# Optimization experiments

Measured on AMD Instinct MI355X. Metric: run time of the kernel, lower is better.

Reference implementation:

```python
import jax, jax.numpy as jnp
import numpy as np

N, E, D_IN, D_H, D_OUT = 100000, 1600000, 128, 128, 47
BN_EPS = 1e-5


def setup_inputs() -> dict:
    key = jax.random.key(0)
    ks = jax.random.split(key, 12)
    x = jax.random.normal(ks[0], (N, D_IN), dtype=jnp.float32)
    edge_index = jax.random.randint(ks[1], (2, E), 0, N, dtype=jnp.int64)
    s = 1.0 / np.sqrt(D_H)
    return {
        "x": x,
        "edge_index": edge_index,
        "W1": jax.random.normal(ks[2], (D_IN, D_H), dtype=jnp.float32) * s,
        "b1": jnp.zeros((D_H,), dtype=jnp.float32),
        "gamma": jax.random.uniform(ks[3], (D_H,), dtype=jnp.float32, minval=0.5, maxval=1.5),
        "beta": jax.random.normal(ks[4], (D_H,), dtype=jnp.float32) * 0.1,
        "mean": jax.random.normal(ks[5], (D_H,), dtype=jnp.float32) * 0.1,
        "var": jax.random.uniform(ks[6], (D_H,), dtype=jnp.float32, minval=0.5, maxval=1.5),
        "W2": jax.random.normal(ks[7], (D_H, D_H), dtype=jnp.float32) * s,
        "b2": jnp.zeros((D_H,), dtype=jnp.float32),
        "Wf": jax.random.normal(ks[8], (D_H, D_OUT), dtype=jnp.float32) * s,
        "bf": jnp.zeros((D_OUT,), dtype=jnp.float32),
    }


def gcn_conv(x, src, dst, W, b, n):
    # x' = x @ W, then symmetric-normalized aggregation with self-loops (PyG GCNConv).
    h = x @ W
    loops = jnp.arange(n, dtype=src.dtype)
    s = jnp.concatenate([src, loops])
    d = jnp.concatenate([dst, loops])
    deg = jax.ops.segment_sum(jnp.ones_like(d, dtype=h.dtype), d, num_segments=n)
    dinv = jnp.where(deg > 0, jax.lax.rsqrt(deg), 0.0)
    norm = dinv[s] * dinv[d]                      # [E+N]
    msg = h[s] * norm[:, None]                    # [E+N, D] gather
    out = jax.ops.segment_sum(msg, d, num_segments=n)  # scatter-add
    return out + b


def reference(x, edge_index, W1, b1, gamma, beta, mean, var, W2, b2, Wf, bf):
    n = x.shape[0]
    src, dst = edge_index[0], edge_index[1]
    # layer 1: GCNConv -> BatchNorm (eval) -> ReLU -> dropout (identity in eval)
    h1 = gcn_conv(x, src, dst, W1, b1, n)
    h1 = (h1 - mean) * jax.lax.rsqrt(var + BN_EPS) * gamma + beta
    h1 = jax.nn.relu(h1)
    # layer 2 (last conv, no BN/act)
    h2 = gcn_conv(h1, src, dst, W2, b2, n)
    # JumpingKnowledge max over layer outputs
    jk = jnp.maximum(h1, h2)
    logits = jk @ Wf + bf
    return jax.nn.log_softmax(logits, axis=1)
```

## Files before the change

kernel.cpp:

```cpp
#include <hip/hip_runtime.h>
#include <math.h>

#define DH 128
#define DOUT 47
#define BN_EPS 1e-5f

typedef __attribute__((ext_vector_type(8))) short short8;
typedef __attribute__((ext_vector_type(4))) float float4v;

__device__ __forceinline__ unsigned bf16_rne(float f) {
    unsigned u = __float_as_uint(f);
    return (u + 0x7fffu + ((u >> 16) & 1u)) >> 16;
}
__device__ __forceinline__ unsigned pack_bf2(float a, float b) {
    return (bf16_rne(a) & 0xffffu) | (bf16_rne(b) << 16);
}
__device__ __forceinline__ float2 unpack_bf2(unsigned u) {
    return make_float2(__uint_as_float(u << 16),
                       __uint_as_float(u & 0xffff0000u));
}


__global__ void zero_int_k(int* __restrict__ p, int n) {
    int i = blockIdx.x * 256 + threadIdx.x;
    if (i < n) p[i] = 0;
}

__global__ __launch_bounds__(256) void count_rank_k(const int* __restrict__ dst,
                                                    int* __restrict__ counts,
                                                    int* __restrict__ rank, int e) {
    int i0 = (blockIdx.x * 256 + threadIdx.x) * 4;
    if (i0 + 4 <= e) {
        int4 d4 = *(const int4*)(dst + i0);
        int4 r4;
        r4.x = atomicAdd(&counts[d4.x], 1);
        r4.y = atomicAdd(&counts[d4.y], 1);
        r4.z = atomicAdd(&counts[d4.z], 1);
        r4.w = atomicAdd(&counts[d4.w], 1);
        *(int4*)(rank + i0) = r4;
    } else {
        for (int i = i0; i < e; i++) rank[i] = atomicAdd(&counts[dst[i]], 1);
    }
}

__global__ __launch_bounds__(256) void scan1_k(const int* __restrict__ counts,
                                               int* __restrict__ offsets,
                                               int* __restrict__ blocksums, int n) {
    __shared__ int sd[256];
    int tid = threadIdx.x;
    int base = blockIdx.x * 1024 + tid * 4;
    int v0 = (base + 0 < n) ? ((counts[base + 0] + 7) & ~7) : 0;
    int v1 = (base + 1 < n) ? ((counts[base + 1] + 7) & ~7) : 0;
    int v2 = (base + 2 < n) ? ((counts[base + 2] + 7) & ~7) : 0;
    int v3 = (base + 3 < n) ? ((counts[base + 3] + 7) & ~7) : 0;
    int tsum = v0 + v1 + v2 + v3;
    sd[tid] = tsum;
    __syncthreads();
    for (int off = 1; off < 256; off <<= 1) {
        int x = (tid >= off) ? sd[tid - off] : 0;
        __syncthreads();
        sd[tid] += x;
        __syncthreads();
    }
    if (tid == 255) blocksums[blockIdx.x] = sd[255];
    int run = sd[tid] - tsum;
    if (base + 0 < n) offsets[base + 0] = run;  run += v0;
    if (base + 1 < n) offsets[base + 1] = run;  run += v1;
    if (base + 2 < n) offsets[base + 2] = run;  run += v2;
    if (base + 3 < n) offsets[base + 3] = run;
}

__global__ __launch_bounds__(128) void scan2_k(int* __restrict__ blocksums, int nb) {
    __shared__ int sd[128];
    int tid = threadIdx.x;
    int v = (tid < nb) ? blocksums[tid] : 0;
    sd[tid] = v;
    __syncthreads();
    for (int off = 1; off < 128; off <<= 1) {
        int x = (tid >= off) ? sd[tid - off] : 0;
        __syncthreads();
        sd[tid] += x;
        __syncthreads();
    }
    if (tid < nb) blocksums[tid] = sd[tid] - v;
}

__global__ void finalize_k(int* __restrict__ offsets,
                           float* __restrict__ dinv, const int* __restrict__ counts,
                           const int* __restrict__ blocksums,
                           int2* __restrict__ ew, int n) {
    int i = blockIdx.x * 256 + threadIdx.x;
    if (i >= n) return;
    int o = offsets[i] + blocksums[i >> 10];
    offsets[i] = o;
    int c = counts[i];
    dinv[i] = rsqrtf((float)(c + 1));
    int cP = (c + 7) & ~7;
    int2 z; z.x = 0; z.y = 0;
    for (int j = o + c; j < o + cP; ++j) ew[j] = z;
}

__global__ __launch_bounds__(256) void scatter_k(const int* __restrict__ src,
                                                 const int* __restrict__ dst,
                                                 const int* __restrict__ rank,
                                                 const int* __restrict__ offsets,
                                                 const float* __restrict__ dinv,
                                                 int2* __restrict__ ew, int e) {
    int i0 = (blockIdx.x * 256 + threadIdx.x) * 4;
    if (i0 + 4 <= e) {
        int4 s4 = *(const int4*)(src + i0);
        int4 d4 = *(const int4*)(dst + i0);
        int4 r4 = *(const int4*)(rank + i0);
        int sa[4] = {s4.x, s4.y, s4.z, s4.w};
        int da[4] = {d4.x, d4.y, d4.z, d4.w};
        int ra[4] = {r4.x, r4.y, r4.z, r4.w};
        int slot[4];
        float w[4];
#pragma unroll
        for (int k = 0; k < 4; k++) slot[k] = offsets[da[k]] + ra[k];
#pragma unroll
        for (int k = 0; k < 4; k++) w[k] = dinv[sa[k]] * dinv[da[k]];
#pragma unroll
        for (int k = 0; k < 4; k++) {
            int2 r; r.x = sa[k]; r.y = __float_as_int(w[k]);
            ew[slot[k]] = r;
        }
    } else {
        for (int i = i0; i < e; i++) {
            int s = src[i], d = dst[i];
            int2 r; r.x = s; r.y = __float_as_int(dinv[s] * dinv[d]);
            ew[offsets[d] + rank[i]] = r;
        }
    }
}

__global__ __launch_bounds__(256) void wprep_k(const float* __restrict__ W1,
                                               const float* __restrict__ W2,
                                               unsigned* __restrict__ W1b,
                                               unsigned* __restrict__ W2b) {
    const float* W = blockIdx.x ? W2 : W1;
    unsigned* Wb = blockIdx.x ? W2b : W1b;
    int tid = threadIdx.x;
    for (int p = tid; p < 128 * 32; p += 256) {
        int n = p >> 5;
        int k0 = (p & 31) << 2;
        float f0 = W[(size_t)(k0 + 0) * 128 + n];
        float f1 = W[(size_t)(k0 + 1) * 128 + n];
        float f2 = W[(size_t)(k0 + 2) * 128 + n];
        float f3 = W[(size_t)(k0 + 3) * 128 + n];
        uint2 v;
        v.x = pack_bf2(f0, f1);
        v.y = pack_bf2(f2, f3);
        *(uint2*)(Wb + (size_t)n * 64 + (k0 >> 1)) = v;
    }
}

__global__ __launch_bounds__(256) void gemm_mfma_k(const float* __restrict__ A,
                                                   const unsigned* __restrict__ Wb,
                                                   unsigned* __restrict__ Cb, int M) {
    __shared__ ushort Bl[128 * 136];
    int tid = threadIdx.x;
    {
        unsigned* Bu = (unsigned*)Bl;
        for (int q = tid; q < 128 * 16; q += 256) {
            int row = q >> 4;
            int c = (q & 15) << 2;
            uint4 v = *(const uint4*)(Wb + (size_t)row * 64 + c);
            *(uint4*)(Bu + (size_t)row * 68 + c) = v;
        }
    }
    __syncthreads();

    int lane = tid & 63;
    int wv = tid >> 6;
    int quad = lane >> 4;
    int l15 = lane & 15;
    int r0 = blockIdx.x * 64 + wv * 16;
    int mload = r0 + l15;
    if (mload > M - 1) mload = M - 1;
    const float* Ar = A + (size_t)mload * 128 + quad * 8;

    float4v acc[8];
#pragma unroll
    for (int t = 0; t < 8; t++) acc[t] = (float4v){0.f, 0.f, 0.f, 0.f};

    for (int kp = 0; kp < 4; ++kp) {
        float4 a0 = *(const float4*)(Ar + kp * 32);
        float4 a1 = *(const float4*)(Ar + kp * 32 + 4);
        float af[8] = {a0.x, a0.y, a0.z, a0.w, a1.x, a1.y, a1.z, a1.w};
        short8 hi, lo;
#pragma unroll
        for (int j = 0; j < 8; j++) {
            unsigned h = bf16_rne(af[j]);
            hi[j] = (short)h;
            float res = af[j] - __uint_as_float(h << 16);
            lo[j] = (short)bf16_rne(res);
        }
        int kb = kp * 32 + quad * 8;
#pragma unroll
        for (int nt = 0; nt < 8; nt++) {
            short8 b8 = *(const short8*)(&Bl[(size_t)(nt * 16 + l15) * 136 + kb]);
            acc[nt] = __builtin_amdgcn_mfma_f32_16x16x32_bf16(hi, b8, acc[nt], 0, 0, 0);
            acc[nt] = __builtin_amdgcn_mfma_f32_16x16x32_bf16(lo, b8, acc[nt], 0, 0, 0);
        }
    }

    ushort* Cu = (ushort*)Cb;
#pragma unroll
    for (int r = 0; r < 4; r++) {
        int row = r0 + quad * 4 + r;
        if (row < M) {
#pragma unroll
            for (int nt = 0; nt < 8; nt++) {
                Cu[(size_t)row * 128 + nt * 16 + l15] = (ushort)bf16_rne(acc[nt][r]);
            }
        }
    }
}

__global__ __launch_bounds__(256) void gemm_bf16_k(const unsigned* __restrict__ Ab,
                                                   const unsigned* __restrict__ Wb,
                                                   unsigned* __restrict__ Cb, int M) {
    __shared__ ushort Bl[128 * 136];
    int tid = threadIdx.x;
    {
        unsigned* Bu = (unsigned*)Bl;
        for (int q = tid; q < 128 * 16; q += 256) {
            int row = q >> 4;
            int c = (q & 15) << 2;
            uint4 v = *(const uint4*)(Wb + (size_t)row * 64 + c);
            *(uint4*)(Bu + (size_t)row * 68 + c) = v;
        }
    }
    __syncthreads();

    int lane = tid & 63;
    int wv = tid >> 6;
    int quad = lane >> 4;
    int l15 = lane & 15;
    int r0 = blockIdx.x * 64 + wv * 16;
    int mload = r0 + l15;
    if (mload > M - 1) mload = M - 1;
    const unsigned* Ar = Ab + (size_t)mload * 64 + quad * 4;

    float4v acc[8];
#pragma unroll
    for (int t = 0; t < 8; t++) acc[t] = (float4v){0.f, 0.f, 0.f, 0.f};

    for (int kp = 0; kp < 4; ++kp) {
        uint4 a4 = *(const uint4*)(Ar + kp * 16);
        short8 av;
        av[0] = (short)(a4.x & 0xffff); av[1] = (short)(a4.x >> 16);
        av[2] = (short)(a4.y & 0xffff); av[3] = (short)(a4.y >> 16);
        av[4] = (short)(a4.z & 0xffff); av[5] = (short)(a4.z >> 16);
        av[6] = (short)(a4.w & 0xffff); av[7] = (short)(a4.w >> 16);
        int kb = kp * 32 + quad * 8;
#pragma unroll
        for (int nt = 0; nt < 8; nt++) {
            short8 b8 = *(const short8*)(&Bl[(size_t)(nt * 16 + l15) * 136 + kb]);
            acc[nt] = __builtin_amdgcn_mfma_f32_16x16x32_bf16(av, b8, acc[nt], 0, 0, 0);
        }
    }

    ushort* Cu = (ushort*)Cb;
#pragma unroll
    for (int r = 0; r < 4; r++) {
        int row = r0 + quad * 4 + r;
        if (row < M) {
#pragma unroll
            for (int nt = 0; nt < 8; nt++) {
                Cu[(size_t)row * 128 + nt * 16 + l15] = (ushort)bf16_rne(acc[nt][r]);
            }
        }
    }
}

__device__ __forceinline__ float4 agg_core(const uint2* __restrict__ Hu2,
                                           const int2* __restrict__ ew,
                                           int start, int cnt, int node,
                                           int li, int half, float di) {
    float4 acc = make_float4(0.f, 0.f, 0.f, 0.f);
    int groups = ((cnt + 7) & ~7) >> 3;
    if (groups > 0) {
        const int2* p = ew + start + half;
        int2 r[4];
#pragma unroll
        for (int k = 0; k < 4; k++) r[k] = p[2 * k];
        for (int g = 0; g < groups; ++g) {
            uint2 gb[4];
#pragma unroll
            for (int k = 0; k < 4; k++)
                gb[k] = Hu2[(size_t)r[k].x * 32 + li];
            int2 rn[4];
            const int2* pn = p + 8 * (g + 1);
#pragma unroll
            for (int k = 0; k < 4; k++) rn[k] = pn[2 * k];
#pragma unroll
            for (int k = 0; k < 4; k++) {
                float w = __int_as_float(r[k].y);
                float2 f0 = unpack_bf2(gb[k].x);
                float2 f1 = unpack_bf2(gb[k].y);
                acc.x = fmaf(f0.x, w, acc.x);
                acc.y = fmaf(f0.y, w, acc.y);
                acc.z = fmaf(f1.x, w, acc.z);
                acc.w = fmaf(f1.y, w, acc.w);
            }
#pragma unroll
            for (int k = 0; k < 4; k++) r[k] = rn[k];
        }
    }
    acc.x += __shfl_xor(acc.x, 32);
    acc.y += __shfl_xor(acc.y, 32);
    acc.z += __shfl_xor(acc.z, 32);
    acc.w += __shfl_xor(acc.w, 32);
    uint2 sv = Hu2[(size_t)node * 32 + li];
    float ws = di * di;
    float2 s0 = unpack_bf2(sv.x);
    float2 s1 = unpack_bf2(sv.y);
    acc.x = fmaf(s0.x, ws, acc.x);
    acc.y = fmaf(s0.y, ws, acc.y);
    acc.z = fmaf(s1.x, ws, acc.z);
    acc.w = fmaf(s1.y, ws, acc.w);
    return acc;
}

__global__ __launch_bounds__(256) void agg1_k(
    const unsigned* __restrict__ H, const int2* __restrict__ ew,
    const int* __restrict__ offsets, const int* __restrict__ counts,
    const float* __restrict__ dinv, const float* __restrict__ b1,
    const float* __restrict__ gamma, const float* __restrict__ beta,
    const float* __restrict__ mean, const float* __restrict__ var,
    unsigned* __restrict__ H1b, int n) {
    int lane = threadIdx.x & 63;
    int li = lane & 31;
    int half = lane >> 5;
    int node = blockIdx.x * 4 + (threadIdx.x >> 6);
    if (node >= n) return;
    float4 acc = agg_core((const uint2*)H, ew, offsets[node], counts[node],
                          node, li, half, dinv[node]);
    if (half == 0) {
        int f0 = li * 4;
        float4 bb = *(const float4*)(b1 + f0);
        float4 mm = *(const float4*)(mean + f0);
        float4 vv = *(const float4*)(var + f0);
        float4 gg = *(const float4*)(gamma + f0);
        float4 be = *(const float4*)(beta + f0);
        float4 o;
        o.x = fmaxf((acc.x + bb.x - mm.x) * rsqrtf(vv.x + BN_EPS) * gg.x + be.x, 0.f);
        o.y = fmaxf((acc.y + bb.y - mm.y) * rsqrtf(vv.y + BN_EPS) * gg.y + be.y, 0.f);
        o.z = fmaxf((acc.z + bb.z - mm.z) * rsqrtf(vv.z + BN_EPS) * gg.z + be.z, 0.f);
        o.w = fmaxf((acc.w + bb.w - mm.w) * rsqrtf(vv.w + BN_EPS) * gg.w + be.w, 0.f);
        uint2 pk;
        pk.x = pack_bf2(o.x, o.y);
        pk.y = pack_bf2(o.z, o.w);
        *(uint2*)(H1b + (size_t)node * 64 + li * 2) = pk;
    }
}

__global__ __launch_bounds__(256) void agg2_k(
    const unsigned* __restrict__ H, const int2* __restrict__ ew,
    const int* __restrict__ offsets, const int* __restrict__ counts,
    const float* __restrict__ dinv, const float* __restrict__ b2,
    unsigned* __restrict__ H1b, int n) {
    int lane = threadIdx.x & 63;
    int li = lane & 31;
    int half = lane >> 5;
    int node = blockIdx.x * 4 + (threadIdx.x >> 6);
    if (node >= n) return;
    float4 acc = agg_core((const uint2*)H, ew, offsets[node], counts[node],
                          node, li, half, dinv[node]);
    if (half == 0) {
        int f0 = li * 4;
        float4 bb = *(const float4*)(b2 + f0);
        uint2* p = (uint2*)(H1b + (size_t)node * 64 + li * 2);
        uint2 hv = *p;
        float2 ha = unpack_bf2(hv.x);
        float2 hb = unpack_bf2(hv.y);
        float4 o;
        o.x = fmaxf(ha.x, acc.x + bb.x);
        o.y = fmaxf(ha.y, acc.y + bb.y);
        o.z = fmaxf(hb.x, acc.z + bb.z);
        o.w = fmaxf(hb.y, acc.w + bb.w);
        uint2 pk;
        pk.x = pack_bf2(o.x, o.y);
        pk.y = pack_bf2(o.z, o.w);
        *p = pk;
    }
}

__global__ __launch_bounds__(256) void head_k(const unsigned* __restrict__ JKb,
                                              const float* __restrict__ Wf,
                                              const float* __restrict__ bf,
                                              float* __restrict__ out, int n) {
    __shared__ __align__(16) float Bs[48 * 132];
    __shared__ __align__(16) float As[64 * 36];
    int tid = threadIdx.x;
    for (int p = tid; p < 47 * 32; p += 256) {
        int c = p >> 5;
        int k0 = (p & 31) << 2;
        float4 v;
        v.x = Wf[(size_t)(k0 + 0) * DOUT + c];
        v.y = Wf[(size_t)(k0 + 1) * DOUT + c];
        v.z = Wf[(size_t)(k0 + 2) * DOUT + c];
        v.w = Wf[(size_t)(k0 + 3) * DOUT + c];
        *(float4*)(&Bs[c * 132 + k0]) = v;
    }
    int tx = tid & 15;
    int ty = tid >> 4;
    int node0 = blockIdx.x * 64;

    float acc[4][3];
#pragma unroll
    for (int i = 0; i < 4; i++)
#pragma unroll
        for (int j = 0; j < 3; j++) acc[i][j] = 0.f;

    for (int kk = 0; kk < 128; kk += 32) {
        __syncthreads();
        for (int l = tid; l < 512; l += 256) {
            int r = l >> 3;
            int c4 = (l & 7) << 2;
            int row = node0 + r;
            float4 v = make_float4(0.f, 0.f, 0.f, 0.f);
            if (row < n) {
                uint2 u = *(const uint2*)(JKb + (size_t)row * 64 + ((kk + c4) >> 1));
                float2 f0 = unpack_bf2(u.x);
                float2 f1 = unpack_bf2(u.y);
                v = make_float4(f0.x, f0.y, f1.x, f1.y);
            }
            *(float4*)(&As[r * 36 + c4]) = v;
        }
        __syncthreads();
#pragma unroll
        for (int k4 = 0; k4 < 32; k4 += 4) {
            float4 a0 = *(const float4*)(&As[(ty * 4 + 0) * 36 + k4]);
            float4 a1 = *(const float4*)(&As[(ty * 4 + 1) * 36 + k4]);
            float4 a2 = *(const float4*)(&As[(ty * 4 + 2) * 36 + k4]);
            float4 a3 = *(const float4*)(&As[(ty * 4 + 3) * 36 + k4]);
            float4 b0 = *(const float4*)(&Bs[(tx * 3 + 0) * 132 + kk + k4]);
            float4 b1 = *(const float4*)(&Bs[(tx * 3 + 1) * 132 + kk + k4]);
            float4 b2 = *(const float4*)(&Bs[(tx * 3 + 2) * 132 + kk + k4]);
#define DOT_ROW(i, a)                                                        \
            acc[i][0] = fmaf(a.x, b0.x, acc[i][0]);                          \
            acc[i][0] = fmaf(a.y, b0.y, acc[i][0]);                          \
            acc[i][0] = fmaf(a.z, b0.z, acc[i][0]);                          \
            acc[i][0] = fmaf(a.w, b0.w, acc[i][0]);                          \
            acc[i][1] = fmaf(a.x, b1.x, acc[i][1]);                          \
            acc[i][1] = fmaf(a.y, b1.y, acc[i][1]);                          \
            acc[i][1] = fmaf(a.z, b1.z, acc[i][1]);                          \
            acc[i][1] = fmaf(a.w, b1.w, acc[i][1]);                          \
            acc[i][2] = fmaf(a.x, b2.x, acc[i][2]);                          \
            acc[i][2] = fmaf(a.y, b2.y, acc[i][2]);                          \
            acc[i][2] = fmaf(a.z, b2.z, acc[i][2]);                          \
            acc[i][2] = fmaf(a.w, b2.w, acc[i][2]);
            DOT_ROW(0, a0)
            DOT_ROW(1, a1)
            DOT_ROW(2, a2)
            DOT_ROW(3, a3)
#undef DOT_ROW
        }
    }

    float bfv[3];
#pragma unroll
    for (int j = 0; j < 3; j++) {
        int c = tx * 3 + j;
        bfv[j] = (c < DOUT) ? bf[c] : 0.f;
    }
#pragma unroll
    for (int i = 0; i < 4; i++) {
        int node = node0 + ty * 4 + i;
        float l0 = acc[i][0] + bfv[0];
        float l1 = acc[i][1] + bfv[1];
        float l2 = acc[i][2] + bfv[2];
        bool v2ok = (tx * 3 + 2) < DOUT;
        float m = fmaxf(l0, l1);
        if (v2ok) m = fmaxf(m, l2);
        for (int off = 8; off >= 1; off >>= 1) m = fmaxf(m, __shfl_xor(m, off));
        float s = expf(l0 - m) + expf(l1 - m) + (v2ok ? expf(l2 - m) : 0.f);
        for (int off = 8; off >= 1; off >>= 1) s += __shfl_xor(s, off);
        float ls = m + logf(s);
        if (node < n) {
            float* o = out + (size_t)node * DOUT + tx * 3;
            o[0] = l0 - ls;
            o[1] = l1 - ls;
            if (v2ok) o[2] = l2 - ls;
        }
    }
}

extern "C" void kernel_launch(void* const* d_in, const int* in_sizes, int n_in,
                              void* d_out, int out_size, void* d_ws, size_t ws_size,
                              hipStream_t stream) {
    const float* x     = (const float*)d_in[0];
    const int*   ei    = (const int*)d_in[1];
    const float* W1    = (const float*)d_in[2];
    const float* b1    = (const float*)d_in[3];
    const float* gamma = (const float*)d_in[4];
    const float* beta  = (const float*)d_in[5];
    const float* mean  = (const float*)d_in[6];
    const float* var   = (const float*)d_in[7];
    const float* W2    = (const float*)d_in[8];
    const float* b2    = (const float*)d_in[9];
    const float* Wf    = (const float*)d_in[10];
    const float* bf    = (const float*)d_in[11];
    float* out = (float*)d_out;

    int N_ = in_sizes[0] / 128;
    int E_ = in_sizes[1] / 2;
    const int* src = ei;
    const int* dst = ei + E_;

    char* ws = (char*)d_ws;
    unsigned* bufA = (unsigned*)ws; ws += (size_t)N_ * 64 * 4;
    unsigned* h1b  = (unsigned*)ws; ws += (size_t)N_ * 64 * 4;
    int*   counts  = (int*)ws;    ws += (size_t)N_ * 4;
    int*   offsets = (int*)ws;    ws += (size_t)N_ * 4;
    float* dinv    = (float*)ws;  ws += (size_t)N_ * 4;
    int*   rank    = (int*)ws;    ws += (size_t)E_ * 4;
    int2*  ew      = (int2*)ws;   ws += ((size_t)E_ + 7 * (size_t)N_ + 64) * 8;
    int*   bsums   = (int*)ws;    ws += 1024 * 4;
    unsigned* W1b  = (unsigned*)ws; ws += 128 * 64 * 4;
    unsigned* W2b  = (unsigned*)ws; ws += 128 * 64 * 4;

    int nb = (N_ + 1023) / 1024;
    int gemmBlocks = (N_ + 63) / 64;
    int edgeBlocks = (E_ + 1023) / 1024;

    zero_int_k<<<(N_ + 255) / 256, 256, 0, stream>>>(counts, N_);
    wprep_k<<<2, 256, 0, stream>>>(W1, W2, W1b, W2b);
    count_rank_k<<<edgeBlocks, 256, 0, stream>>>(dst, counts, rank, E_);
    scan1_k<<<nb, 256, 0, stream>>>(counts, offsets, bsums, N_);
    scan2_k<<<1, 128, 0, stream>>>(bsums, nb);
    finalize_k<<<(N_ + 255) / 256, 256, 0, stream>>>(offsets, dinv,
                                                     counts, bsums, ew, N_);
    scatter_k<<<edgeBlocks, 256, 0, stream>>>(src, dst, rank, offsets, dinv, ew, E_);

    gemm_mfma_k<<<gemmBlocks, 256, 0, stream>>>(x, W1b, bufA, N_);
    agg1_k<<<(N_ + 3) / 4, 256, 0, stream>>>(bufA, ew, offsets, counts, dinv,
                                             b1, gamma, beta, mean, var, h1b, N_);
    gemm_bf16_k<<<gemmBlocks, 256, 0, stream>>>(h1b, W2b, bufA, N_);
    agg2_k<<<(N_ + 3) / 4, 256, 0, stream>>>(bufA, ew, offsets, counts, dinv,
                                             b2, h1b, N_);
    head_k<<<(N_ + 63) / 64, 256, 0, stream>>>(h1b, Wf, bf, out, N_);
}
```

Before: 461.3 us.

## Factor GCN normalization into GEMM epilogue and store source-only edge lists

Splits the symmetric normalization dinv[s]*dinv[d] so the source factor is applied in the GEMM epilogue and the destination factor after aggregation. The CSR edge list then holds only source indices (4 bytes instead of 8), which cuts edge-list traffic in scatter and both aggregations. Padding slots point at a zeroed sentinel row appended to the feature buffer. The zero and weight-prep kernels are merged into one launch. Pre-scaling by dinv before the bf16 rounding changes rounding slightly.

Result: faster. 425.0 us (-7.9%).

```diff
diff --git a/kernel.cpp b/kernel.cpp
--- a/kernel.cpp
+++ b/kernel.cpp
@@ -21,9 +21,33 @@
 }
 
 
-__global__ void zero_int_k(int* __restrict__ p, int n) {
-    int i = blockIdx.x * 256 + threadIdx.x;
-    if (i < n) p[i] = 0;
+__global__ __launch_bounds__(256) void prep_k(const float* __restrict__ W1,
+                                              const float* __restrict__ W2,
+                                              unsigned* __restrict__ W1b,
+                                              unsigned* __restrict__ W2b,
+                                              int* __restrict__ counts,
+                                              unsigned* __restrict__ bufA, int n) {
+    int tid = threadIdx.x;
+    if (blockIdx.x >= 2) {
+        int i = (blockIdx.x - 2) * 256 + tid;
+        if (i < n) counts[i] = 0;
+        return;
+    }
+    const float* W = blockIdx.x ? W2 : W1;
+    unsigned* Wb = blockIdx.x ? W2b : W1b;
+    if (blockIdx.x == 0 && tid < 64) bufA[(size_t)n * 64 + tid] = 0;
+    for (int p = tid; p < 128 * 32; p += 256) {
+        int nn = p >> 5;
+        int k0 = (p & 31) << 2;
+        float f0 = W[(size_t)(k0 + 0) * 128 + nn];
+        float f1 = W[(size_t)(k0 + 1) * 128 + nn];
+        float f2 = W[(size_t)(k0 + 2) * 128 + nn];
+        float f3 = W[(size_t)(k0 + 3) * 128 + nn];
+        uint2 v;
+        v.x = pack_bf2(f0, f1);
+        v.y = pack_bf2(f2, f3);
+        *(uint2*)(Wb + (size_t)nn * 64 + (k0 >> 1)) = v;
+    }
 }
 
 __global__ __launch_bounds__(256) void count_rank_k(const int* __restrict__ dst,
@@ -88,7 +112,7 @@
 __global__ void finalize_k(int* __restrict__ offsets,
                            float* __restrict__ dinv, const int* __restrict__ counts,
                            const int* __restrict__ blocksums,
-                           int2* __restrict__ ew, int n) {
+                           int* __restrict__ el, int n) {
     int i = blockIdx.x * 256 + threadIdx.x;
     if (i >= n) return;
     int o = offsets[i] + blocksums[i >> 10];
@@ -96,67 +120,31 @@
     int c = counts[i];
     dinv[i] = rsqrtf((float)(c + 1));
     int cP = (c + 7) & ~7;
-    int2 z; z.x = 0; z.y = 0;
-    for (int j = o + c; j < o + cP; ++j) ew[j] = z;
+    for (int j = o + c; j < o + cP; ++j) el[j] = n;
 }
 
 __global__ __launch_bounds__(256) void scatter_k(const int* __restrict__ src,
                                                  const int* __restrict__ dst,
                                                  const int* __restrict__ rank,
                                                  const int* __restrict__ offsets,
-                                                 const float* __restrict__ dinv,
-                                                 int2* __restrict__ ew, int e) {
+                                                 int* __restrict__ el, int e) {
     int i0 = (blockIdx.x * 256 + threadIdx.x) * 4;
     if (i0 + 4 <= e) {
         int4 s4 = *(const int4*)(src + i0);
         int4 d4 = *(const int4*)(dst + i0);
         int4 r4 = *(const int4*)(rank + i0);
-        int sa[4] = {s4.x, s4.y, s4.z, s4.w};
-        int da[4] = {d4.x, d4.y, d4.z, d4.w};
-        int ra[4] = {r4.x, r4.y, r4.z, r4.w};
-        int slot[4];
-        float w[4];
-#pragma unroll
-        for (int k = 0; k < 4; k++) slot[k] = offsets[da[k]] + ra[k];
-#pragma unroll
-        for (int k = 0; k < 4; k++) w[k] = dinv[sa[k]] * dinv[da[k]];
-#pragma unroll
-        for (int k = 0; k < 4; k++) {
-            int2 r; r.x = sa[k]; r.y = __float_as_int(w[k]);
-            ew[slot[k]] = r;
-        }
+        el[offsets[d4.x] + r4.x] = s4.x;
+        el[offsets[d4.y] + r4.y] = s4.y;
+        el[offsets[d4.z] + r4.z] = s4.z;
+        el[offsets[d4.w] + r4.w] = s4.w;
     } else {
-        for (int i = i0; i < e; i++) {
-            int s = src[i], d = dst[i];
-            int2 r; r.x = s; r.y = __float_as_int(dinv[s] * dinv[d]);
-            ew[offsets[d] + rank[i]] = r;
-        }
-    }
-}
-
-__global__ __launch_bounds__(256) void wprep_k(const float* __restrict__ W1,
-                                               const float* __restrict__ W2,
-                                               unsigned* __restrict__ W1b,
-                                               unsigned* __restrict__ W2b) {
-    const float* W = blockIdx.x ? W2 : W1;
-    unsigned* Wb = blockIdx.x ? W2b : W1b;
-    int tid = threadIdx.x;
-    for (int p = tid; p < 128 * 32; p += 256) {
-        int n = p >> 5;
-        int k0 = (p & 31) << 2;
-        float f0 = W[(size_t)(k0 + 0) * 128 + n];
-        float f1 = W[(size_t)(k0 + 1) * 128 + n];
-        float f2 = W[(size_t)(k0 + 2) * 128 + n];
-        float f3 = W[(size_t)(k0 + 3) * 128 + n];
-        uint2 v;
-        v.x = pack_bf2(f0, f1);
-        v.y = pack_bf2(f2, f3);
-        *(uint2*)(Wb + (size_t)n * 64 + (k0 >> 1)) = v;
+        for (int i = i0; i < e; i++) el[offsets[dst[i]] + rank[i]] = src[i];
     }
 }
 
 __global__ __launch_bounds__(256) void gemm_mfma_k(const float* __restrict__ A,
                                                    const unsigned* __restrict__ Wb,
+                                                   const float* __restrict__ dinv,
                                                    unsigned* __restrict__ Cb, int M) {
     __shared__ ushort Bl[128 * 136];
     int tid = threadIdx.x;
@@ -210,9 +198,11 @@
     for (int r = 0; r < 4; r++) {
         int row = r0 + quad * 4 + r;
         if (row < M) {
+            float dv = dinv[row];
 #pragma unroll
             for (int nt = 0; nt < 8; nt++) {
-                Cu[(size_t)row * 128 + nt * 16 + l15] = (ushort)bf16_rne(acc[nt][r]);
+                Cu[(size_t)row * 128 + nt * 16 + l15] =
+                    (ushort)bf16_rne(acc[nt][r] * dv);
             }
         }
     }
@@ -220,6 +210,7 @@
 
 __global__ __launch_bounds__(256) void gemm_bf16_k(const unsigned* __restrict__ Ab,
                                                    const unsigned* __restrict__ Wb,
+                                                   const float* __restrict__ dinv,
                                                    unsigned* __restrict__ Cb, int M) {
     __shared__ ushort Bl[128 * 136];
     int tid = threadIdx.x;
@@ -267,46 +258,41 @@
     for (int r = 0; r < 4; r++) {
         int row = r0 + quad * 4 + r;
         if (row < M) {
+            float dv = dinv[row];
 #pragma unroll
             for (int nt = 0; nt < 8; nt++) {
-                Cu[(size_t)row * 128 + nt * 16 + l15] = (ushort)bf16_rne(acc[nt][r]);
+                Cu[(size_t)row * 128 + nt * 16 + l15] =
+                    (ushort)bf16_rne(acc[nt][r] * dv);
             }
         }
     }
 }
 
 __device__ __forceinline__ float4 agg_core(const uint2* __restrict__ Hu2,
-                                           const int2* __restrict__ ew,
+                                           const int* __restrict__ el,
                                            int start, int cnt, int node,
-                                           int li, int half, float di) {
+                                           int li, int half) {
     float4 acc = make_float4(0.f, 0.f, 0.f, 0.f);
     int groups = ((cnt + 7) & ~7) >> 3;
     if (groups > 0) {
-        const int2* p = ew + start + half;
-        int2 r[4];
-#pragma unroll
-        for (int k = 0; k < 4; k++) r[k] = p[2 * k];
+        const int* p = el + start + half * 4;
+        int4 r = *(const int4*)p;
         for (int g = 0; g < groups; ++g) {
-            uint2 gb[4];
-#pragma unroll
-            for (int k = 0; k < 4; k++)
-                gb[k] = Hu2[(size_t)r[k].x * 32 + li];
-            int2 rn[4];
-            const int2* pn = p + 8 * (g + 1);
-#pragma unroll
-            for (int k = 0; k < 4; k++) rn[k] = pn[2 * k];
-#pragma unroll
-            for (int k = 0; k < 4; k++) {
-                float w = __int_as_float(r[k].y);
-                float2 f0 = unpack_bf2(gb[k].x);
-                float2 f1 = unpack_bf2(gb[k].y);
-                acc.x = fmaf(f0.x, w, acc.x);
-                acc.y = fmaf(f0.y, w, acc.y);
-                acc.z = fmaf(f1.x, w, acc.z);
-                acc.w = fmaf(f1.y, w, acc.w);
-            }
-#pragma unroll
-            for (int k = 0; k < 4; k++) r[k] = rn[k];
+            uint2 g0 = Hu2[(size_t)r.x * 32 + li];
+            uint2 g1 = Hu2[(size_t)r.y * 32 + li];
+            uint2 g2 = Hu2[(size_t)r.z * 32 + li];
+            uint2 g3 = Hu2[(size_t)r.w * 32 + li];
+            int4 rn = *(const int4*)(p + 8 * (g + 1));
+            float2 f;
+            f = unpack_bf2(g0.x); acc.x += f.x; acc.y += f.y;
+            f = unpack_bf2(g0.y); acc.z += f.x; acc.w += f.y;
+            f = unpack_bf2(g1.x); acc.x += f.x; acc.y += f.y;
+            f = unpack_bf2(g1.y); acc.z += f.x; acc.w += f.y;
+            f = unpack_bf2(g2.x); acc.x += f.x; acc.y += f.y;
+            f = unpack_bf2(g2.y); acc.z += f.x; acc.w += f.y;
+            f = unpack_bf2(g3.x); acc.x += f.x; acc.y += f.y;
+            f = unpack_bf2(g3.y); acc.z += f.x; acc.w += f.y;
+            r = rn;
         }
     }
     acc.x += __shfl_xor(acc.x, 32);
@@ -314,18 +300,14 @@
     acc.z += __shfl_xor(acc.z, 32);
     acc.w += __shfl_xor(acc.w, 32);
     uint2 sv = Hu2[(size_t)node * 32 + li];
-    float ws = di * di;
     float2 s0 = unpack_bf2(sv.x);
     float2 s1 = unpack_bf2(sv.y);
-    acc.x = fmaf(s0.x, ws, acc.x);
-    acc.y = fmaf(s0.y, ws, acc.y);
-    acc.z = fmaf(s1.x, ws, acc.z);
-    acc.w = fmaf(s1.y, ws, acc.w);
+    acc.x += s0.x; acc.y += s0.y; acc.z += s1.x; acc.w += s1.y;
     return acc;
 }
 
 __global__ __launch_bounds__(256) void agg1_k(
-    const unsigned* __restrict__ H, const int2* __restrict__ ew,
+    const unsigned* __restrict__ H, const int* __restrict__ el,
     const int* __restrict__ offsets, const int* __restrict__ counts,
     const float* __restrict__ dinv, const float* __restrict__ b1,
     const float* __restrict__ gamma, const float* __restrict__ beta,
@@ -336,9 +318,10 @@
     int half = lane >> 5;
     int node = blockIdx.x * 4 + (threadIdx.x >> 6);
     if (node >= n) return;
-    float4 acc = agg_core((const uint2*)H, ew, offsets[node], counts[node],
-                          node, li, half, dinv[node]);
+    float4 acc = agg_core((const uint2*)H, el, offsets[node], counts[node],
+                          node, li, half);
     if (half == 0) {
+        float dv = dinv[node];
         int f0 = li * 4;
         float4 bb = *(const float4*)(b1 + f0);
         float4 mm = *(const float4*)(mean + f0);
@@ -346,10 +329,10 @@
         float4 gg = *(const float4*)(gamma + f0);
         float4 be = *(const float4*)(beta + f0);
         float4 o;
-        o.x = fmaxf((acc.x + bb.x - mm.x) * rsqrtf(vv.x + BN_EPS) * gg.x + be.x, 0.f);
-        o.y = fmaxf((acc.y + bb.y - mm.y) * rsqrtf(vv.y + BN_EPS) * gg.y + be.y, 0.f);
-        o.z = fmaxf((acc.z + bb.z - mm.z) * rsqrtf(vv.z + BN_EPS) * gg.z + be.z, 0.f);
-        o.w = fmaxf((acc.w + bb.w - mm.w) * rsqrtf(vv.w + BN_EPS) * gg.w + be.w, 0.f);
+        o.x = fmaxf((acc.x * dv + bb.x - mm.x) * rsqrtf(vv.x + BN_EPS) * gg.x + be.x, 0.f);
+        o.y = fmaxf((acc.y * dv + bb.y - mm.y) * rsqrtf(vv.y + BN_EPS) * gg.y + be.y, 0.f);
+        o.z = fmaxf((acc.z * dv + bb.z - mm.z) * rsqrtf(vv.z + BN_EPS) * gg.z + be.z, 0.f);
+        o.w = fmaxf((acc.w * dv + bb.w - mm.w) * rsqrtf(vv.w + BN_EPS) * gg.w + be.w, 0.f);
         uint2 pk;
         pk.x = pack_bf2(o.x, o.y);
         pk.y = pack_bf2(o.z, o.w);
@@ -358,7 +341,7 @@
 }
 
 __global__ __launch_bounds__(256) void agg2_k(
-    const unsigned* __restrict__ H, const int2* __restrict__ ew,
+    const unsigned* __restrict__ H, const int* __restrict__ el,
     const int* __restrict__ offsets, const int* __restrict__ counts,
     const float* __restrict__ dinv, const float* __restrict__ b2,
     unsigned* __restrict__ H1b, int n) {
@@ -367,9 +350,10 @@
     int half = lane >> 5;
     int node = blockIdx.x * 4 + (threadIdx.x >> 6);
     if (node >= n) return;
-    float4 acc = agg_core((const uint2*)H, ew, offsets[node], counts[node],
-                          node, li, half, dinv[node]);
+    float4 acc = agg_core((const uint2*)H, el, offsets[node], counts[node],
+                          node, li, half);
     if (half == 0) {
+        float dv = dinv[node];
         int f0 = li * 4;
         float4 bb = *(const float4*)(b2 + f0);
         uint2* p = (uint2*)(H1b + (size_t)node * 64 + li * 2);
@@ -377,10 +361,10 @@
         float2 ha = unpack_bf2(hv.x);
         float2 hb = unpack_bf2(hv.y);
         float4 o;
-        o.x = fmaxf(ha.x, acc.x + bb.x);
-        o.y = fmaxf(ha.y, acc.y + bb.y);
-        o.z = fmaxf(hb.x, acc.z + bb.z);
-        o.w = fmaxf(hb.y, acc.w + bb.w);
+        o.x = fmaxf(ha.x, acc.x * dv + bb.x);
+        o.y = fmaxf(ha.y, acc.y * dv + bb.y);
+        o.z = fmaxf(hb.x, acc.z * dv + bb.z);
+        o.w = fmaxf(hb.y, acc.w * dv + bb.w);
         uint2 pk;
         pk.x = pack_bf2(o.x, o.y);
         pk.y = pack_bf2(o.z, o.w);
@@ -512,13 +496,13 @@
     const int* dst = ei + E_;
 
     char* ws = (char*)d_ws;
-    unsigned* bufA = (unsigned*)ws; ws += (size_t)N_ * 64 * 4;
+    unsigned* bufA = (unsigned*)ws; ws += (size_t)(N_ + 1) * 64 * 4;
     unsigned* h1b  = (unsigned*)ws; ws += (size_t)N_ * 64 * 4;
     int*   counts  = (int*)ws;    ws += (size_t)N_ * 4;
     int*   offsets = (int*)ws;    ws += (size_t)N_ * 4;
     float* dinv    = (float*)ws;  ws += (size_t)N_ * 4;
     int*   rank    = (int*)ws;    ws += (size_t)E_ * 4;
-    int2*  ew      = (int2*)ws;   ws += ((size_t)E_ + 7 * (size_t)N_ + 64) * 8;
+    int*   el      = (int*)ws;    ws += ((size_t)E_ + 7 * (size_t)N_ + 16) * 4;
     int*   bsums   = (int*)ws;    ws += 1024 * 4;
     unsigned* W1b  = (unsigned*)ws; ws += 128 * 64 * 4;
     unsigned* W2b  = (unsigned*)ws; ws += 128 * 64 * 4;
@@ -527,20 +511,20 @@
     int gemmBlocks = (N_ + 63) / 64;
     int edgeBlocks = (E_ + 1023) / 1024;
 
-    zero_int_k<<<(N_ + 255) / 256, 256, 0, stream>>>(counts, N_);
-    wprep_k<<<2, 256, 0, stream>>>(W1, W2, W1b, W2b);
+    prep_k<<<2 + (N_ + 255) / 256, 256, 0, stream>>>(W1, W2, W1b, W2b,
+                                                     counts, bufA, N_);
     count_rank_k<<<edgeBlocks, 256, 0, stream>>>(dst, counts, rank, E_);
     scan1_k<<<nb, 256, 0, stream>>>(counts, offsets, bsums, N_);
     scan2_k<<<1, 128, 0, stream>>>(bsums, nb);
     finalize_k<<<(N_ + 255) / 256, 256, 0, stream>>>(offsets, dinv,
-                                                     counts, bsums, ew, N_);
-    scatter_k<<<edgeBlocks, 256, 0, stream>>>(src, dst, rank, offsets, dinv, ew, E_);
-
-    gemm_mfma_k<<<gemmBlocks, 256, 0, stream>>>(x, W1b, bufA, N_);
-    agg1_k<<<(N_ + 3) / 4, 256, 0, stream>>>(bufA, ew, offsets, counts, dinv,
+                                                     counts, bsums, el, N_);
+    scatter_k<<<edgeBlocks, 256, 0, stream>>>(src, dst, rank, offsets, el, E_);
+
+    gemm_mfma_k<<<gemmBlocks, 256, 0, stream>>>(x, W1b, dinv, bufA, N_);
+    agg1_k<<<(N_ + 3) / 4, 256, 0, stream>>>(bufA, el, offsets, counts, dinv,
                                              b1, gamma, beta, mean, var, h1b, N_);
-    gemm_bf16_k<<<gemmBlocks, 256, 0, stream>>>(h1b, W2b, bufA, N_);
-    agg2_k<<<(N_ + 3) / 4, 256, 0, stream>>>(bufA, ew, offsets, counts, dinv,
+    gemm_bf16_k<<<gemmBlocks, 256, 0, stream>>>(h1b, W2b, dinv, bufA, N_);
+    agg2_k<<<(N_ + 3) / 4, 256, 0, stream>>>(bufA, el, offsets, counts, dinv,
                                              b2, h1b, N_);
     head_k<<<(N_ + 63) / 64, 256, 0, stream>>>(h1b, Wf, bf, out, N_);
 }
```
